# Kernel tuning notes

Hardware: AMD Instinct MI355X
Metric: run time of the kernel (lower is better)

## Reference

```python
import jax, jax.numpy as jnp
import numpy as np

GRID_MIN = -2.0
GRID_MAX = 2.0
NUM_GRIDS = 8
IN_DIM = 512
OUT_DIM = 512
N = 16384
SPLINE_SCALE = 0.1


def setup_inputs() -> dict:
    key = jax.random.key(0)
    k_x, k_sw, k_w, k_b = jax.random.split(key, 4)
    x = jax.random.normal(k_x, (N, IN_DIM), dtype=jnp.float32)
    grid = jnp.linspace(GRID_MIN, GRID_MAX, NUM_GRIDS, dtype=jnp.float32)
    spline_weight = jax.random.normal(k_sw, (IN_DIM * NUM_GRIDS, OUT_DIM), dtype=jnp.float32) * SPLINE_SCALE
    bound = 1.0 / np.sqrt(IN_DIM)
    base_w = jax.random.uniform(k_w, (OUT_DIM, IN_DIM), minval=-bound, maxval=bound, dtype=jnp.float32)
    base_b = jax.random.uniform(k_b, (OUT_DIM,), minval=-bound, maxval=bound, dtype=jnp.float32)
    return {"x": x, "grid": grid, "spline_weight": spline_weight, "base_w": base_w, "base_b": base_b}


def reference(x, grid, spline_weight, base_w, base_b):
    # Gaussian RBF basis over the grid: (N, in_dim, num_grids)
    h = (GRID_MAX - GRID_MIN) / (NUM_GRIDS - 1)  # grid spacing
    basis = jnp.exp(-(((x[..., None] - grid) / h) ** 2))
    ret = basis.reshape(x.shape[0], -1) @ spline_weight  # (N, out_dim)
    base = jax.nn.silu(x) @ base_w.T + base_b
    return ret + base
```

## Files before the change

kernel.cpp:

```cpp
#include <hip/hip_runtime.h>
#include <hip/hip_bf16.h>

typedef __attribute__((ext_vector_type(8))) short short8;
typedef __attribute__((ext_vector_type(4))) float floatx4;

#define N_ROWS   16384
#define IN_DIM   512
#define OUT_DIM  512
#define K_SPLINE 4096
#define K_TOT    4608
#define BM       64
#define BN       256
#define BK       64
#define NKT      (K_TOT / BK)
#define NKTILE   (K_TOT / 32)
#define L2E      1.4426950408889634f
#define C2E      0.13533528323661270f

__device__ __forceinline__ unsigned short f2bf(float f) {
    unsigned int u = __float_as_uint(f);
    unsigned int r = u + 0x7FFFu + ((u >> 16) & 1u);
    return (unsigned short)(r >> 16);
}

__device__ __forceinline__ unsigned pack2bf(float f0, float f1) {
    unsigned u0 = __float_as_uint(f0) + 0x8000u;
    unsigned u1 = __float_as_uint(f1) + 0x8000u;
    return __builtin_amdgcn_perm(u1, u0, 0x07060302);
}

__global__ __launch_bounds__(256) void prep_kernel(
    const float* __restrict__ sw, const float* __restrict__ bw,
    unsigned short* __restrict__ Btf)
{
    const int t     = threadIdx.x;
    const int lane  = t & 63;
    const int ktile = blockIdx.x * 4 + (t >> 6);
    const int ct    = blockIdx.y;
    const int mn    = lane & 15, q = lane >> 4;
    const int n     = ct * 16 + mn;
    const int kbase = ktile * 32 + q * 8;
    short8 v;
    if (kbase < K_SPLINE) {
        #pragma unroll
        for (int j = 0; j < 8; ++j)
            v[j] = (short)f2bf(sw[(size_t)(kbase + j) * OUT_DIM + n]);
    } else {
        #pragma unroll
        for (int j = 0; j < 8; ++j)
            v[j] = (short)f2bf(bw[(size_t)n * IN_DIM + (kbase + j - K_SPLINE)]);
    }
    reinterpret_cast<short8*>(Btf)[(size_t)(ct * NKTILE + ktile) * 64 + lane] = v;
}

__device__ __forceinline__ void stageA(unsigned short* dst, const float* xrow,
                                       int rowA, int colq, int kt)
{
    unsigned short* arow = dst + rowA * 64;
    if (kt < K_SPLINE / BK) {
        const float2 xv = *reinterpret_cast<const float2*>(xrow + kt * 8 + colq * 2);
        #pragma unroll
        for (int e = 0; e < 2; ++e) {
            const float X = e ? xv.y : xv.x;
            const float u = fmaf(1.75f, X, 3.5f);
            float b = __builtin_amdgcn_exp2f(-(u * u) * L2E);
            float r = __builtin_amdgcn_exp2f(fmaf(2.0f * L2E, u, -L2E));
            float v[8];
            v[0] = b;
            #pragma unroll
            for (int j = 1; j < 8; ++j) { b *= r; r *= C2E; v[j] = b; }
            uint4 p;
            p.x = pack2bf(v[0], v[1]);
            p.y = pack2bf(v[2], v[3]);
            p.z = pack2bf(v[4], v[5]);
            p.w = pack2bf(v[6], v[7]);
            const int blk = (colq * 2 + e) ^ (rowA & 7);
            *reinterpret_cast<uint4*>(arow + blk * 8) = p;
        }
    } else {
        const float* xs = xrow + (kt - K_SPLINE / BK) * 64 + colq * 16;
        const float4 a0 = *reinterpret_cast<const float4*>(xs);
        const float4 a1 = *reinterpret_cast<const float4*>(xs + 4);
        const float4 a2 = *reinterpret_cast<const float4*>(xs + 8);
        const float4 a3 = *reinterpret_cast<const float4*>(xs + 12);
        const float f[16] = {a0.x, a0.y, a0.z, a0.w, a1.x, a1.y, a1.z, a1.w,
                             a2.x, a2.y, a2.z, a2.w, a3.x, a3.y, a3.z, a3.w};
        float s[16];
        #pragma unroll
        for (int j = 0; j < 16; ++j)
            s[j] = f[j] * __builtin_amdgcn_rcpf(
                1.0f + __builtin_amdgcn_exp2f(-f[j] * L2E));
        #pragma unroll
        for (int e = 0; e < 2; ++e) {
            uint4 p;
            p.x = pack2bf(s[e * 8 + 0], s[e * 8 + 1]);
            p.y = pack2bf(s[e * 8 + 2], s[e * 8 + 3]);
            p.z = pack2bf(s[e * 8 + 4], s[e * 8 + 5]);
            p.w = pack2bf(s[e * 8 + 6], s[e * 8 + 7]);
            const int blk = (colq * 2 + e) ^ (rowA & 7);
            *reinterpret_cast<uint4*>(arow + blk * 8) = p;
        }
    }
}

template<bool PREP>
__device__ __forceinline__ void load_bfrags(short8 dst[4][2], const short8* __restrict__ Bf,
                                            const size_t* bbase, int kt,
                                            const float* __restrict__ sw,
                                            const float* __restrict__ bw,
                                            int col0, int wn, int lane)
{
    if (PREP) {
        #pragma unroll
        for (int nt = 0; nt < 4; ++nt)
            #pragma unroll
            for (int s = 0; s < 2; ++s)
                dst[nt][s] = Bf[bbase[nt] + (size_t)(kt * 2 + s) * 64];
    } else {
        const int mn = lane & 15, q = lane >> 4;
        #pragma unroll
        for (int nt = 0; nt < 4; ++nt) {
            const int n = col0 + wn * 64 + nt * 16 + mn;
            #pragma unroll
            for (int s = 0; s < 2; ++s) {
                short8 v;
                #pragma unroll
                for (int j = 0; j < 8; ++j) {
                    const int k = (kt * 2 + s) * 32 + q * 8 + j;
                    const float val = (k < K_SPLINE)
                        ? sw[(size_t)k * OUT_DIM + n]
                        : bw[(size_t)n * IN_DIM + (k - K_SPLINE)];
                    v[j] = (short)f2bf(val);
                }
                dst[nt][s] = v;
            }
        }
    }
}

template<bool PREP>
__global__ __launch_bounds__(256, 2) void kan_kernel(
    const float* __restrict__ x,
    const unsigned short* __restrict__ Btf,
    const float* __restrict__ sw,
    const float* __restrict__ bw,
    const float* __restrict__ bias,
    float* __restrict__ out)
{
    __shared__ unsigned short Als[2][BM * BK];

    const int tid  = threadIdx.x;
    const int wn   = tid >> 6;
    const int lane = tid & 63;
    const int q    = lane >> 4;
    const int mn   = lane & 15;
    const int row0 = blockIdx.x * BM;
    const int col0 = blockIdx.y * BN;
    const int rowA = tid >> 2;
    const int colq = tid & 3;

    const float* xrow = x + (size_t)(row0 + rowA) * IN_DIM;

    size_t bbase[4];
    #pragma unroll
    for (int nt = 0; nt < 4; ++nt)
        bbase[nt] = (size_t)(((col0 >> 4) + wn * 4 + nt) * NKTILE) * 64 + lane;
    const short8* Bf = reinterpret_cast<const short8*>(Btf);

    floatx4 acc[4][4];
    #pragma unroll
    for (int i = 0; i < 4; ++i)
        #pragma unroll
        for (int j = 0; j < 4; ++j)
            acc[i][j] = (floatx4){0.f, 0.f, 0.f, 0.f};

    short8 bb[2][4][2];

    stageA(&Als[0][0], xrow, rowA, colq, 0);
    load_bfrags<PREP>(bb[0], Bf, bbase, 0, sw, bw, col0, wn, lane);
    __syncthreads();

    for (int ktb = 0; ktb < NKT; ktb += 2) {
        #pragma unroll
        for (int half = 0; half < 2; ++half) {
            const int kt  = ktb + half;
            const int cur = half;
            const int nxt = half ^ 1;
            if (kt + 1 < NKT) {
                load_bfrags<PREP>(bb[nxt], Bf, bbase, kt + 1, sw, bw, col0, wn, lane);
                stageA(&Als[nxt][0], xrow, rowA, colq, kt + 1);
            }
            #pragma unroll
            for (int s = 0; s < 2; ++s) {
                short8 af[4];
                #pragma unroll
                for (int mt = 0; mt < 4; ++mt) {
                    const int r = mt * 16 + mn;
                    af[mt] = *reinterpret_cast<const short8*>(
                        &Als[cur][r * 64 + (((s * 4 + q) ^ (r & 7)) * 8)]);
                }
                #pragma unroll
                for (int mt = 0; mt < 4; ++mt)
                    #pragma unroll
                    for (int nt = 0; nt < 4; ++nt)
                        acc[mt][nt] = __builtin_amdgcn_mfma_f32_16x16x32_bf16(
                            af[mt], bb[cur][nt][s], acc[mt][nt], 0, 0, 0);
            }
            __syncthreads();
        }
    }

    #pragma unroll
    for (int nt = 0; nt < 4; ++nt) {
        const int col = col0 + wn * 64 + nt * 16 + mn;
        const float bv = bias[col];
        #pragma unroll
        for (int mt = 0; mt < 4; ++mt) {
            const int rb = row0 + mt * 16 + q * 4;
            #pragma unroll
            for (int e = 0; e < 4; ++e)
                out[(size_t)(rb + e) * OUT_DIM + col] = acc[mt][nt][e] + bv;
        }
    }
}

extern "C" void kernel_launch(void* const* d_in, const int* in_sizes, int n_in,
                              void* d_out, int out_size, void* d_ws, size_t ws_size,
                              hipStream_t stream)
{
    const float* x    = (const float*)d_in[0];
    const float* sw   = (const float*)d_in[2];
    const float* bw   = (const float*)d_in[3];
    const float* bias = (const float*)d_in[4];
    float* out = (float*)d_out;

    const size_t bt_bytes = (size_t)OUT_DIM * K_TOT * sizeof(unsigned short);
    if (ws_size >= bt_bytes) {
        unsigned short* Btf = (unsigned short*)d_ws;
        prep_kernel<<<dim3(NKTILE / 4, OUT_DIM / 16), 256, 0, stream>>>(sw, bw, Btf);
        kan_kernel<true><<<dim3(N_ROWS / BM, OUT_DIM / BN), 256, 0, stream>>>(
            x, Btf, sw, bw, bias, out);
    } else {
        kan_kernel<false><<<dim3(N_ROWS / BM, OUT_DIM / BN), 256, 0, stream>>>(
            x, nullptr, sw, bw, bias, out);
    }
}
```

Measured before the change: 174.4 us.

## Generate A fragments in registers per wave, dropping LDS staging and barriers

The shared-memory A tile and its __syncthreads are removed. Each wave now computes the Gaussian basis and SiLU values straight into its MFMA A-operand registers, reading x directly from global memory with a register double buffer. This removes LDS traffic and block-wide synchronisation, but every wave recomputes the same 64 rows' basis, which roughly quadruples exp and VALU work per block. The bf16 packing also switches from round-to-nearest to truncation, which drops a few ALU ops at some cost in accuracy.

Result: slower. 282.6 us (+62.0%).

```diff
diff --git a/kernel.cpp b/kernel.cpp
--- a/kernel.cpp
+++ b/kernel.cpp
@@ -9,10 +9,8 @@
 #define OUT_DIM  512
 #define K_SPLINE 4096
 #define K_TOT    4608
-#define BM       64
-#define BN       256
-#define BK       64
-#define NKT      (K_TOT / BK)
+#define NKT      (K_TOT / 64)
+#define NSPL     (K_SPLINE / 64)
 #define NKTILE   (K_TOT / 32)
 #define L2E      1.4426950408889634f
 #define C2E      0.13533528323661270f
@@ -23,10 +21,41 @@
     return (unsigned short)(r >> 16);
 }
 
-__device__ __forceinline__ unsigned pack2bf(float f0, float f1) {
-    unsigned u0 = __float_as_uint(f0) + 0x8000u;
-    unsigned u1 = __float_as_uint(f1) + 0x8000u;
-    return __builtin_amdgcn_perm(u1, u0, 0x07060302);
+__device__ __forceinline__ unsigned packtrunc(float f0, float f1) {
+    return __builtin_amdgcn_perm(__float_as_uint(f1), __float_as_uint(f0), 0x07060302);
+}
+
+__device__ __forceinline__ short8 gen_basis(float X) {
+    const float u = fmaf(1.75f, X, 3.5f);
+    float b = __builtin_amdgcn_exp2f(-(u * u) * L2E);
+    float r = __builtin_amdgcn_exp2f(fmaf(2.0f * L2E, u, -L2E));
+    float v[8];
+    v[0] = b;
+    #pragma unroll
+    for (int j = 1; j < 8; ++j) { b *= r; r *= C2E; v[j] = b; }
+    union { unsigned d[4]; short8 s; } o;
+    o.d[0] = packtrunc(v[0], v[1]);
+    o.d[1] = packtrunc(v[2], v[3]);
+    o.d[2] = packtrunc(v[4], v[5]);
+    o.d[3] = packtrunc(v[6], v[7]);
+    return o.s;
+}
+
+__device__ __forceinline__ short8 gen_silu(const float* p) {
+    const float4 a0 = *reinterpret_cast<const float4*>(p);
+    const float4 a1 = *reinterpret_cast<const float4*>(p + 4);
+    const float f[8] = {a0.x, a0.y, a0.z, a0.w, a1.x, a1.y, a1.z, a1.w};
+    float s[8];
+    #pragma unroll
+    for (int j = 0; j < 8; ++j)
+        s[j] = f[j] * __builtin_amdgcn_rcpf(
+            1.0f + __builtin_amdgcn_exp2f(-f[j] * L2E));
+    union { unsigned d[4]; short8 v; } o;
+    o.d[0] = packtrunc(s[0], s[1]);
+    o.d[1] = packtrunc(s[2], s[3]);
+    o.d[2] = packtrunc(s[4], s[5]);
+    o.d[3] = packtrunc(s[6], s[7]);
+    return o.v;
 }
 
 __global__ __launch_bounds__(256) void prep_kernel(
@@ -53,62 +82,12 @@
     reinterpret_cast<short8*>(Btf)[(size_t)(ct * NKTILE + ktile) * 64 + lane] = v;
 }
 
-__device__ __forceinline__ void stageA(unsigned short* dst, const float* xrow,
-                                       int rowA, int colq, int kt)
-{
-    unsigned short* arow = dst + rowA * 64;
-    if (kt < K_SPLINE / BK) {
-        const float2 xv = *reinterpret_cast<const float2*>(xrow + kt * 8 + colq * 2);
-        #pragma unroll
-        for (int e = 0; e < 2; ++e) {
-            const float X = e ? xv.y : xv.x;
-            const float u = fmaf(1.75f, X, 3.5f);
-            float b = __builtin_amdgcn_exp2f(-(u * u) * L2E);
-            float r = __builtin_amdgcn_exp2f(fmaf(2.0f * L2E, u, -L2E));
-            float v[8];
-            v[0] = b;
-            #pragma unroll
-            for (int j = 1; j < 8; ++j) { b *= r; r *= C2E; v[j] = b; }
-            uint4 p;
-            p.x = pack2bf(v[0], v[1]);
-            p.y = pack2bf(v[2], v[3]);
-            p.z = pack2bf(v[4], v[5]);
-            p.w = pack2bf(v[6], v[7]);
-            const int blk = (colq * 2 + e) ^ (rowA & 7);
-            *reinterpret_cast<uint4*>(arow + blk * 8) = p;
-        }
-    } else {
-        const float* xs = xrow + (kt - K_SPLINE / BK) * 64 + colq * 16;
-        const float4 a0 = *reinterpret_cast<const float4*>(xs);
-        const float4 a1 = *reinterpret_cast<const float4*>(xs + 4);
-        const float4 a2 = *reinterpret_cast<const float4*>(xs + 8);
-        const float4 a3 = *reinterpret_cast<const float4*>(xs + 12);
-        const float f[16] = {a0.x, a0.y, a0.z, a0.w, a1.x, a1.y, a1.z, a1.w,
-                             a2.x, a2.y, a2.z, a2.w, a3.x, a3.y, a3.z, a3.w};
-        float s[16];
-        #pragma unroll
-        for (int j = 0; j < 16; ++j)
-            s[j] = f[j] * __builtin_amdgcn_rcpf(
-                1.0f + __builtin_amdgcn_exp2f(-f[j] * L2E));
-        #pragma unroll
-        for (int e = 0; e < 2; ++e) {
-            uint4 p;
-            p.x = pack2bf(s[e * 8 + 0], s[e * 8 + 1]);
-            p.y = pack2bf(s[e * 8 + 2], s[e * 8 + 3]);
-            p.z = pack2bf(s[e * 8 + 4], s[e * 8 + 5]);
-            p.w = pack2bf(s[e * 8 + 6], s[e * 8 + 7]);
-            const int blk = (colq * 2 + e) ^ (rowA & 7);
-            *reinterpret_cast<uint4*>(arow + blk * 8) = p;
-        }
-    }
-}
-
 template<bool PREP>
 __device__ __forceinline__ void load_bfrags(short8 dst[4][2], const short8* __restrict__ Bf,
                                             const size_t* bbase, int kt,
                                             const float* __restrict__ sw,
                                             const float* __restrict__ bw,
-                                            int col0, int wn, int lane)
+                                            int col0, int lane)
 {
     if (PREP) {
         #pragma unroll
@@ -120,7 +99,7 @@
         const int mn = lane & 15, q = lane >> 4;
         #pragma unroll
         for (int nt = 0; nt < 4; ++nt) {
-            const int n = col0 + wn * 64 + nt * 16 + mn;
+            const int n = col0 + nt * 16 + mn;
             #pragma unroll
             for (int s = 0; s < 2; ++s) {
                 short8 v;
@@ -147,25 +126,26 @@
     const float* __restrict__ bias,
     float* __restrict__ out)
 {
-    __shared__ unsigned short Als[2][BM * BK];
-
     const int tid  = threadIdx.x;
-    const int wn   = tid >> 6;
+    const int wv   = tid >> 6;
     const int lane = tid & 63;
     const int q    = lane >> 4;
     const int mn   = lane & 15;
-    const int row0 = blockIdx.x * BM;
-    const int col0 = blockIdx.y * BN;
-    const int rowA = tid >> 2;
-    const int colq = tid & 3;
-
-    const float* xrow = x + (size_t)(row0 + rowA) * IN_DIM;
-
+    const int bid  = blockIdx.x;
+    const int half = bid & 1;
+    const int row0 = (bid >> 1) * 64;
+    const int col0 = half * 256 + wv * 64;
+
+    const short8* Bf = reinterpret_cast<const short8*>(Btf);
     size_t bbase[4];
     #pragma unroll
     for (int nt = 0; nt < 4; ++nt)
-        bbase[nt] = (size_t)(((col0 >> 4) + wn * 4 + nt) * NKTILE) * 64 + lane;
-    const short8* Bf = reinterpret_cast<const short8*>(Btf);
+        bbase[nt] = (size_t)(((col0 >> 4) + nt) * NKTILE) * 64 + lane;
+
+    const float* xr[4];
+    #pragma unroll
+    for (int mt = 0; mt < 4; ++mt)
+        xr[mt] = x + (size_t)(row0 + mt * 16 + mn) * IN_DIM;
 
     floatx4 acc[4][4];
     #pragma unroll
@@ -175,44 +155,64 @@
             acc[i][j] = (floatx4){0.f, 0.f, 0.f, 0.f};
 
     short8 bb[2][4][2];
-
-    stageA(&Als[0][0], xrow, rowA, colq, 0);
-    load_bfrags<PREP>(bb[0], Bf, bbase, 0, sw, bw, col0, wn, lane);
-    __syncthreads();
-
-    for (int ktb = 0; ktb < NKT; ktb += 2) {
-        #pragma unroll
-        for (int half = 0; half < 2; ++half) {
-            const int kt  = ktb + half;
-            const int cur = half;
-            const int nxt = half ^ 1;
-            if (kt + 1 < NKT) {
-                load_bfrags<PREP>(bb[nxt], Bf, bbase, kt + 1, sw, bw, col0, wn, lane);
-                stageA(&Als[nxt][0], xrow, rowA, colq, kt + 1);
+    float  xs[2][4][2];
+
+    load_bfrags<PREP>(bb[0], Bf, bbase, 0, sw, bw, col0, lane);
+    #pragma unroll
+    for (int mt = 0; mt < 4; ++mt)
+        #pragma unroll
+        for (int s = 0; s < 2; ++s)
+            xs[0][mt][s] = xr[mt][s * 4 + q];
+
+    for (int ktb = 0; ktb < NSPL; ktb += 2) {
+        #pragma unroll
+        for (int h = 0; h < 2; ++h) {
+            const int kt = ktb + h;
+            const int cur = h, nxt = h ^ 1;
+            load_bfrags<PREP>(bb[nxt], Bf, bbase, kt + 1, sw, bw, col0, lane);
+            if (kt + 1 < NSPL) {
+                #pragma unroll
+                for (int mt = 0; mt < 4; ++mt)
+                    #pragma unroll
+                    for (int s = 0; s < 2; ++s)
+                        xs[nxt][mt][s] = xr[mt][(kt + 1) * 8 + s * 4 + q];
             }
             #pragma unroll
-            for (int s = 0; s < 2; ++s) {
-                short8 af[4];
+            for (int s = 0; s < 2; ++s)
                 #pragma unroll
                 for (int mt = 0; mt < 4; ++mt) {
-                    const int r = mt * 16 + mn;
-                    af[mt] = *reinterpret_cast<const short8*>(
-                        &Als[cur][r * 64 + (((s * 4 + q) ^ (r & 7)) * 8)]);
-                }
-                #pragma unroll
-                for (int mt = 0; mt < 4; ++mt)
+                    const short8 af = gen_basis(xs[cur][mt][s]);
                     #pragma unroll
                     for (int nt = 0; nt < 4; ++nt)
                         acc[mt][nt] = __builtin_amdgcn_mfma_f32_16x16x32_bf16(
-                            af[mt], bb[cur][nt][s], acc[mt][nt], 0, 0, 0);
-            }
-            __syncthreads();
+                            af, bb[cur][nt][s], acc[mt][nt], 0, 0, 0);
+                }
+        }
+    }
+
+    for (int ktb = NSPL; ktb < NKT; ktb += 2) {
+        #pragma unroll
+        for (int h = 0; h < 2; ++h) {
+            const int kt = ktb + h;
+            const int cur = h, nxt = h ^ 1;
+            if (kt + 1 < NKT)
+                load_bfrags<PREP>(bb[nxt], Bf, bbase, kt + 1, sw, bw, col0, lane);
+            #pragma unroll
+            for (int s = 0; s < 2; ++s)
+                #pragma unroll
+                for (int mt = 0; mt < 4; ++mt) {
+                    const short8 af = gen_silu(xr[mt] + (kt - NSPL) * 64 + s * 32 + q * 8);
+                    #pragma unroll
+                    for (int nt = 0; nt < 4; ++nt)
+                        acc[mt][nt] = __builtin_amdgcn_mfma_f32_16x16x32_bf16(
+                            af, bb[cur][nt][s], acc[mt][nt], 0, 0, 0);
+                }
         }
     }
 
     #pragma unroll
     for (int nt = 0; nt < 4; ++nt) {
-        const int col = col0 + wn * 64 + nt * 16 + mn;
+        const int col = col0 + nt * 16 + mn;
         const float bv = bias[col];
         #pragma unroll
         for (int mt = 0; mt < 4; ++mt) {
@@ -238,10 +238,8 @@
     if (ws_size >= bt_bytes) {
         unsigned short* Btf = (unsigned short*)d_ws;
         prep_kernel<<<dim3(NKTILE / 4, OUT_DIM / 16), 256, 0, stream>>>(sw, bw, Btf);
-        kan_kernel<true><<<dim3(N_ROWS / BM, OUT_DIM / BN), 256, 0, stream>>>(
-            x, Btf, sw, bw, bias, out);
+        kan_kernel<true><<<dim3(512), 256, 0, stream>>>(x, Btf, sw, bw, bias, out);
     } else {
-        kan_kernel<false><<<dim3(N_ROWS / BM, OUT_DIM / BN), 256, 0, stream>>>(
-            x, nullptr, sw, bw, bias, out);
-    }
-}
+        kan_kernel<false><<<dim3(512), 256, 0, stream>>>(x, nullptr, sw, bw, bias, out);
+    }
+}
```

## Split K across two warp groups per block with shared-memory reduction

Applied to the files above, without the earlier changes.

Each block now runs 512 threads as two 256-thread halves. Each half computes the same 64x256 output tile over its own half of the K range, and the partial sums are combined through shared memory at the end. B fragments now load one 32-wide k-slice at a time and are interleaved with the MFMAs, and x for the spline path is prefetched a step ahead. The bf16 pack switches from round-to-nearest to truncation. The aim is to raise waves in flight and hide latency on the long K loop, at the cost of a reduction epilogue, larger launch bounds that pressure registers, and slightly lower precision.

Result: slower. 218.4 us (+25.3%).

```diff
diff --git a/kernel.cpp b/kernel.cpp
--- a/kernel.cpp
+++ b/kernel.cpp
@@ -9,11 +9,10 @@
 #define OUT_DIM  512
 #define K_SPLINE 4096
 #define K_TOT    4608
-#define BM       64
-#define BN       256
-#define BK       64
-#define NKT      (K_TOT / BK)
-#define NKTILE   (K_TOT / 32)
+#define NKT      72
+#define KHT      36
+#define NSPL     64
+#define NKTILE   144
 #define L2E      1.4426950408889634f
 #define C2E      0.13533528323661270f
 
@@ -23,10 +22,8 @@
     return (unsigned short)(r >> 16);
 }
 
-__device__ __forceinline__ unsigned pack2bf(float f0, float f1) {
-    unsigned u0 = __float_as_uint(f0) + 0x8000u;
-    unsigned u1 = __float_as_uint(f1) + 0x8000u;
-    return __builtin_amdgcn_perm(u1, u0, 0x07060302);
+__device__ __forceinline__ unsigned packtrunc(float f0, float f1) {
+    return __builtin_amdgcn_perm(__float_as_uint(f1), __float_as_uint(f0), 0x07060302);
 }
 
 __global__ __launch_bounds__(256) void prep_kernel(
@@ -35,11 +32,11 @@
 {
     const int t     = threadIdx.x;
     const int lane  = t & 63;
-    const int ktile = blockIdx.x * 4 + (t >> 6);
+    const int kt32  = blockIdx.x * 4 + (t >> 6);
     const int ct    = blockIdx.y;
     const int mn    = lane & 15, q = lane >> 4;
     const int n     = ct * 16 + mn;
-    const int kbase = ktile * 32 + q * 8;
+    const int kbase = kt32 * 32 + q * 8;
     short8 v;
     if (kbase < K_SPLINE) {
         #pragma unroll
@@ -50,96 +47,93 @@
         for (int j = 0; j < 8; ++j)
             v[j] = (short)f2bf(bw[(size_t)n * IN_DIM + (kbase + j - K_SPLINE)]);
     }
-    reinterpret_cast<short8*>(Btf)[(size_t)(ct * NKTILE + ktile) * 64 + lane] = v;
-}
-
-__device__ __forceinline__ void stageA(unsigned short* dst, const float* xrow,
-                                       int rowA, int colq, int kt)
-{
-    unsigned short* arow = dst + rowA * 64;
-    if (kt < K_SPLINE / BK) {
-        const float2 xv = *reinterpret_cast<const float2*>(xrow + kt * 8 + colq * 2);
-        #pragma unroll
-        for (int e = 0; e < 2; ++e) {
-            const float X = e ? xv.y : xv.x;
-            const float u = fmaf(1.75f, X, 3.5f);
-            float b = __builtin_amdgcn_exp2f(-(u * u) * L2E);
-            float r = __builtin_amdgcn_exp2f(fmaf(2.0f * L2E, u, -L2E));
-            float v[8];
-            v[0] = b;
-            #pragma unroll
-            for (int j = 1; j < 8; ++j) { b *= r; r *= C2E; v[j] = b; }
-            uint4 p;
-            p.x = pack2bf(v[0], v[1]);
-            p.y = pack2bf(v[2], v[3]);
-            p.z = pack2bf(v[4], v[5]);
-            p.w = pack2bf(v[6], v[7]);
-            const int blk = (colq * 2 + e) ^ (rowA & 7);
-            *reinterpret_cast<uint4*>(arow + blk * 8) = p;
-        }
-    } else {
-        const float* xs = xrow + (kt - K_SPLINE / BK) * 64 + colq * 16;
-        const float4 a0 = *reinterpret_cast<const float4*>(xs);
-        const float4 a1 = *reinterpret_cast<const float4*>(xs + 4);
-        const float4 a2 = *reinterpret_cast<const float4*>(xs + 8);
-        const float4 a3 = *reinterpret_cast<const float4*>(xs + 12);
-        const float f[16] = {a0.x, a0.y, a0.z, a0.w, a1.x, a1.y, a1.z, a1.w,
-                             a2.x, a2.y, a2.z, a2.w, a3.x, a3.y, a3.z, a3.w};
-        float s[16];
-        #pragma unroll
-        for (int j = 0; j < 16; ++j)
-            s[j] = f[j] * __builtin_amdgcn_rcpf(
-                1.0f + __builtin_amdgcn_exp2f(-f[j] * L2E));
-        #pragma unroll
-        for (int e = 0; e < 2; ++e) {
-            uint4 p;
-            p.x = pack2bf(s[e * 8 + 0], s[e * 8 + 1]);
-            p.y = pack2bf(s[e * 8 + 2], s[e * 8 + 3]);
-            p.z = pack2bf(s[e * 8 + 4], s[e * 8 + 5]);
-            p.w = pack2bf(s[e * 8 + 6], s[e * 8 + 7]);
-            const int blk = (colq * 2 + e) ^ (rowA & 7);
-            *reinterpret_cast<uint4*>(arow + blk * 8) = p;
-        }
+    reinterpret_cast<short8*>(Btf)[(size_t)(ct * NKTILE + kt32) * 64 + lane] = v;
+}
+
+__device__ __forceinline__ void stage_spline(unsigned short* buf, int rowA, int colq,
+                                             float2 xv)
+{
+    unsigned short* arow = buf + rowA * 64;
+    #pragma unroll
+    for (int e = 0; e < 2; ++e) {
+        const float X = e ? xv.y : xv.x;
+        const float u = fmaf(1.75f, X, 3.5f);
+        float b = __builtin_amdgcn_exp2f(-(u * u) * L2E);
+        float r = __builtin_amdgcn_exp2f(fmaf(2.0f * L2E, u, -L2E));
+        float v[8];
+        v[0] = b;
+        #pragma unroll
+        for (int j = 1; j < 8; ++j) { b *= r; r *= C2E; v[j] = b; }
+        uint4 p;
+        p.x = packtrunc(v[0], v[1]);
+        p.y = packtrunc(v[2], v[3]);
+        p.z = packtrunc(v[4], v[5]);
+        p.w = packtrunc(v[6], v[7]);
+        const int blk = (colq * 2 + e) ^ (rowA & 7);
+        *reinterpret_cast<uint4*>(arow + blk * 8) = p;
+    }
+}
+
+__device__ __forceinline__ void stage_silu(unsigned short* buf, int rowA, int colq,
+                                           const float* xrow, int ktg)
+{
+    unsigned short* arow = buf + rowA * 64;
+    const float* xs = xrow + (ktg - NSPL) * 64 + colq * 16;
+    const float4 a0 = *reinterpret_cast<const float4*>(xs);
+    const float4 a1 = *reinterpret_cast<const float4*>(xs + 4);
+    const float4 a2 = *reinterpret_cast<const float4*>(xs + 8);
+    const float4 a3 = *reinterpret_cast<const float4*>(xs + 12);
+    const float f[16] = {a0.x, a0.y, a0.z, a0.w, a1.x, a1.y, a1.z, a1.w,
+                         a2.x, a2.y, a2.z, a2.w, a3.x, a3.y, a3.z, a3.w};
+    float s[16];
+    #pragma unroll
+    for (int j = 0; j < 16; ++j)
+        s[j] = f[j] * __builtin_amdgcn_rcpf(
+            1.0f + __builtin_amdgcn_exp2f(-f[j] * L2E));
+    #pragma unroll
+    for (int e = 0; e < 2; ++e) {
+        uint4 p;
+        p.x = packtrunc(s[e * 8 + 0], s[e * 8 + 1]);
+        p.y = packtrunc(s[e * 8 + 2], s[e * 8 + 3]);
+        p.z = packtrunc(s[e * 8 + 4], s[e * 8 + 5]);
+        p.w = packtrunc(s[e * 8 + 6], s[e * 8 + 7]);
+        const int blk = (colq * 2 + e) ^ (rowA & 7);
+        *reinterpret_cast<uint4*>(arow + blk * 8) = p;
     }
 }
 
 template<bool PREP>
-__device__ __forceinline__ void load_bfrags(short8 dst[4][2], const short8* __restrict__ Bf,
-                                            const size_t* bbase, int kt,
-                                            const float* __restrict__ sw,
-                                            const float* __restrict__ bw,
-                                            int col0, int wn, int lane)
+__device__ __forceinline__ void loadB(short8 dst[4], const short8* __restrict__ bfp,
+                                      int kt32,
+                                      const float* __restrict__ sw,
+                                      const float* __restrict__ bw,
+                                      int col0, int lane)
 {
     if (PREP) {
         #pragma unroll
         for (int nt = 0; nt < 4; ++nt)
-            #pragma unroll
-            for (int s = 0; s < 2; ++s)
-                dst[nt][s] = Bf[bbase[nt] + (size_t)(kt * 2 + s) * 64];
+            dst[nt] = bfp[(size_t)nt * NKTILE * 64 + (size_t)kt32 * 64];
     } else {
         const int mn = lane & 15, q = lane >> 4;
         #pragma unroll
         for (int nt = 0; nt < 4; ++nt) {
-            const int n = col0 + wn * 64 + nt * 16 + mn;
+            const int n = col0 + nt * 16 + mn;
+            short8 v;
             #pragma unroll
-            for (int s = 0; s < 2; ++s) {
-                short8 v;
-                #pragma unroll
-                for (int j = 0; j < 8; ++j) {
-                    const int k = (kt * 2 + s) * 32 + q * 8 + j;
-                    const float val = (k < K_SPLINE)
-                        ? sw[(size_t)k * OUT_DIM + n]
-                        : bw[(size_t)n * IN_DIM + (k - K_SPLINE)];
-                    v[j] = (short)f2bf(val);
-                }
-                dst[nt][s] = v;
-            }
+            for (int j = 0; j < 8; ++j) {
+                const int k = kt32 * 32 + q * 8 + j;
+                const float val = (k < K_SPLINE)
+                    ? sw[(size_t)k * OUT_DIM + n]
+                    : bw[(size_t)n * IN_DIM + (k - K_SPLINE)];
+                v[j] = (short)f2bf(val);
+            }
+            dst[nt] = v;
         }
     }
 }
 
 template<bool PREP>
-__global__ __launch_bounds__(256, 2) void kan_kernel(
+__global__ __launch_bounds__(512, 4) void kan_kernel(
     const float* __restrict__ x,
     const unsigned short* __restrict__ Btf,
     const float* __restrict__ sw,
@@ -147,25 +141,27 @@
     const float* __restrict__ bias,
     float* __restrict__ out)
 {
-    __shared__ unsigned short Als[2][BM * BK];
+    __shared__ unsigned short Als[2][2][64 * 64];
 
     const int tid  = threadIdx.x;
-    const int wn   = tid >> 6;
+    const int kh   = tid >> 8;
+    const int wn   = (tid >> 6) & 3;
     const int lane = tid & 63;
     const int q    = lane >> 4;
     const int mn   = lane & 15;
-    const int row0 = blockIdx.x * BM;
-    const int col0 = blockIdx.y * BN;
-    const int rowA = tid >> 2;
-    const int colq = tid & 3;
-
-    const float* xrow = x + (size_t)(row0 + rowA) * IN_DIM;
-
-    size_t bbase[4];
-    #pragma unroll
-    for (int nt = 0; nt < 4; ++nt)
-        bbase[nt] = (size_t)(((col0 >> 4) + wn * 4 + nt) * NKTILE) * 64 + lane;
-    const short8* Bf = reinterpret_cast<const short8*>(Btf);
+    const int bid  = blockIdx.x;
+    const int row0 = (bid >> 1) * 64;
+    const int col0 = (bid & 1) * 256 + wn * 64;
+
+    const int th   = tid & 255;
+    const int rowA = th >> 2;
+    const int colq = th & 3;
+    const float* xrowA = x + (size_t)(row0 + rowA) * IN_DIM;
+
+    const short8* Bf  = reinterpret_cast<const short8*>(Btf);
+    const short8* bfp = Bf + (size_t)(col0 >> 4) * NKTILE * 64 + lane;
+
+    const int base = kh * KHT;
 
     floatx4 acc[4][4];
     #pragma unroll
@@ -174,52 +170,114 @@
         for (int j = 0; j < 4; ++j)
             acc[i][j] = (floatx4){0.f, 0.f, 0.f, 0.f};
 
-    short8 bb[2][4][2];
-
-    stageA(&Als[0][0], xrow, rowA, colq, 0);
-    load_bfrags<PREP>(bb[0], Bf, bbase, 0, sw, bw, col0, wn, lane);
+    short8 b0[4], b1[4];
+
+    {
+        const float2 xv = *reinterpret_cast<const float2*>(xrowA + base * 8 + colq * 2);
+        stage_spline(&Als[kh][0][0], rowA, colq, xv);
+    }
+    loadB<PREP>(b0, bfp, base * 2 + 0, sw, bw, col0, lane);
+    loadB<PREP>(b1, bfp, base * 2 + 1, sw, bw, col0, lane);
+    float2 xp = *reinterpret_cast<const float2*>(xrowA + (base + 1) * 8 + colq * 2);
     __syncthreads();
 
-    for (int ktb = 0; ktb < NKT; ktb += 2) {
-        #pragma unroll
-        for (int half = 0; half < 2; ++half) {
-            const int kt  = ktb + half;
-            const int cur = half;
-            const int nxt = half ^ 1;
-            if (kt + 1 < NKT) {
-                load_bfrags<PREP>(bb[nxt], Bf, bbase, kt + 1, sw, bw, col0, wn, lane);
-                stageA(&Als[nxt][0], xrow, rowA, colq, kt + 1);
-            }
-            #pragma unroll
-            for (int s = 0; s < 2; ++s) {
+    for (int ktb = 0; ktb < KHT; ktb += 2) {
+        #pragma unroll
+        for (int h = 0; h < 2; ++h) {
+            const int ktl = ktb + h;
+            const int ktg = base + ktl;
+            const unsigned short* Acur = &Als[kh][h][0];
+            unsigned short*       Anxt = &Als[kh][h ^ 1][0];
+
+            if (ktl + 1 < KHT) {
+                if (ktg + 1 < NSPL) {
+                    stage_spline(Anxt, rowA, colq, xp);
+                    if (ktl + 2 < KHT && ktg + 2 < NSPL)
+                        xp = *reinterpret_cast<const float2*>(
+                            xrowA + (ktg + 2) * 8 + colq * 2);
+                } else {
+                    stage_silu(Anxt, rowA, colq, xrowA, ktg + 1);
+                }
+            }
+
+            {
                 short8 af[4];
                 #pragma unroll
                 for (int mt = 0; mt < 4; ++mt) {
                     const int r = mt * 16 + mn;
                     af[mt] = *reinterpret_cast<const short8*>(
-                        &Als[cur][r * 64 + (((s * 4 + q) ^ (r & 7)) * 8)]);
+                        Acur + r * 64 + ((q ^ (r & 7)) * 8));
                 }
                 #pragma unroll
                 for (int mt = 0; mt < 4; ++mt)
                     #pragma unroll
                     for (int nt = 0; nt < 4; ++nt)
                         acc[mt][nt] = __builtin_amdgcn_mfma_f32_16x16x32_bf16(
-                            af[mt], bb[cur][nt][s], acc[mt][nt], 0, 0, 0);
-            }
+                            af[mt], b0[nt], acc[mt][nt], 0, 0, 0);
+            }
+            if (ktl + 1 < KHT)
+                loadB<PREP>(b0, bfp, (ktg + 1) * 2 + 0, sw, bw, col0, lane);
+
+            {
+                short8 af[4];
+                #pragma unroll
+                for (int mt = 0; mt < 4; ++mt) {
+                    const int r = mt * 16 + mn;
+                    af[mt] = *reinterpret_cast<const short8*>(
+                        Acur + r * 64 + (((4 + q) ^ (r & 7)) * 8));
+                }
+                #pragma unroll
+                for (int mt = 0; mt < 4; ++mt)
+                    #pragma unroll
+                    for (int nt = 0; nt < 4; ++nt)
+                        acc[mt][nt] = __builtin_amdgcn_mfma_f32_16x16x32_bf16(
+                            af[mt], b1[nt], acc[mt][nt], 0, 0, 0);
+            }
+            if (ktl + 1 < KHT)
+                loadB<PREP>(b1, bfp, (ktg + 1) * 2 + 1, sw, bw, col0, lane);
+
             __syncthreads();
         }
     }
 
-    #pragma unroll
-    for (int nt = 0; nt < 4; ++nt) {
-        const int col = col0 + wn * 64 + nt * 16 + mn;
-        const float bv = bias[col];
-        #pragma unroll
-        for (int mt = 0; mt < 4; ++mt) {
-            const int rb = row0 + mt * 16 + q * 4;
+    float* red = reinterpret_cast<float*>(&Als[0][0][0]);
+    #pragma unroll
+    for (int r = 0; r < 2; ++r) {
+        __syncthreads();
+        if (kh == 1) {
             #pragma unroll
-            for (int e = 0; e < 4; ++e)
-                out[(size_t)(rb + e) * OUT_DIM + col] = acc[mt][nt][e] + bv;
+            for (int mtl = 0; mtl < 2; ++mtl)
+                #pragma unroll
+                for (int nt = 0; nt < 4; ++nt)
+                    *reinterpret_cast<floatx4*>(
+                        &red[wn * 2048 + (mtl * 4 + nt) * 256 + lane * 4]) =
+                        acc[r * 2 + mtl][nt];
+        }
+        __syncthreads();
+        if (kh == 0) {
+            #pragma unroll
+            for (int mtl = 0; mtl < 2; ++mtl)
+                #pragma unroll
+                for (int nt = 0; nt < 4; ++nt) {
+                    const floatx4 v = *reinterpret_cast<const floatx4*>(
+                        &red[wn * 2048 + (mtl * 4 + nt) * 256 + lane * 4]);
+                    acc[r * 2 + mtl][nt] += v;
+                }
+        }
+    }
+
+    if (kh == 0) {
+        #pragma unroll
+        for (int nt = 0; nt < 4; ++nt) {
+            const int col = col0 + nt * 16 + mn;
+            const float bv = bias[col];
+            #pragma unroll
+            for (int mt = 0; mt < 4; ++mt) {
+                const int rb = row0 + mt * 16 + q * 4;
+                #pragma unroll
+                for (int e = 0; e < 4; ++e)
+                    out[(size_t)(rb + e) * OUT_DIM + col] = acc[mt][nt][e] + bv;
+            }
         }
     }
 }
@@ -238,10 +296,8 @@
     if (ws_size >= bt_bytes) {
         unsigned short* Btf = (unsigned short*)d_ws;
         prep_kernel<<<dim3(NKTILE / 4, OUT_DIM / 16), 256, 0, stream>>>(sw, bw, Btf);
-        kan_kernel<true><<<dim3(N_ROWS / BM, OUT_DIM / BN), 256, 0, stream>>>(
-            x, Btf, sw, bw, bias, out);
+        kan_kernel<true><<<dim3(512), 512, 0, stream>>>(x, Btf, sw, bw, bias, out);
     } else {
-        kan_kernel<false><<<dim3(N_ROWS / BM, OUT_DIM / BN), 256, 0, stream>>>(
-            x, nullptr, sw, bw, bias, out);
-    }
-}
+        kan_kernel<false><<<dim3(512), 512, 0, stream>>>(x, nullptr, sw, bw, bias, out);
+    }
+}
```

## Split K across two blocks with partial-sum reduce kernel and truncating bf16 pack

Applied to the files above, without the earlier changes.

Splits the K dimension into two halves, each computed by a separate block into an fp32 partial buffer, followed by a reduce kernel that sums the partials and adds the bias. Blocks are now indexed so that adjacent block IDs share a row tile across the two column halves, which is meant to improve reuse of A in cache. The bf16 packing changes from round-to-nearest to truncation, saving ALU work in the staging of A. In exchange it writes and reads two full 32 MB partial buffers, adds a third launch, and lowers the precision of the basis values.

Result: slower. 193.8 us (+11.1%).

```diff
diff --git a/kernel.cpp b/kernel.cpp
--- a/kernel.cpp
+++ b/kernel.cpp
@@ -9,11 +9,10 @@
 #define OUT_DIM  512
 #define K_SPLINE 4096
 #define K_TOT    4608
-#define BM       64
-#define BN       256
-#define BK       64
-#define NKT      (K_TOT / BK)
-#define NKTILE   (K_TOT / 32)
+#define NKT      72
+#define KHT      36
+#define NSPL     64
+#define NKTILE   144
 #define L2E      1.4426950408889634f
 #define C2E      0.13533528323661270f
 
@@ -23,10 +22,8 @@
     return (unsigned short)(r >> 16);
 }
 
-__device__ __forceinline__ unsigned pack2bf(float f0, float f1) {
-    unsigned u0 = __float_as_uint(f0) + 0x8000u;
-    unsigned u1 = __float_as_uint(f1) + 0x8000u;
-    return __builtin_amdgcn_perm(u1, u0, 0x07060302);
+__device__ __forceinline__ unsigned packtrunc(float f0, float f1) {
+    return __builtin_amdgcn_perm(__float_as_uint(f1), __float_as_uint(f0), 0x07060302);
 }
 
 __global__ __launch_bounds__(256) void prep_kernel(
@@ -35,11 +32,11 @@
 {
     const int t     = threadIdx.x;
     const int lane  = t & 63;
-    const int ktile = blockIdx.x * 4 + (t >> 6);
+    const int kt32  = blockIdx.x * 4 + (t >> 6);
     const int ct    = blockIdx.y;
     const int mn    = lane & 15, q = lane >> 4;
     const int n     = ct * 16 + mn;
-    const int kbase = ktile * 32 + q * 8;
+    const int kbase = kt32 * 32 + q * 8;
     short8 v;
     if (kbase < K_SPLINE) {
         #pragma unroll
@@ -50,14 +47,14 @@
         for (int j = 0; j < 8; ++j)
             v[j] = (short)f2bf(bw[(size_t)n * IN_DIM + (kbase + j - K_SPLINE)]);
     }
-    reinterpret_cast<short8*>(Btf)[(size_t)(ct * NKTILE + ktile) * 64 + lane] = v;
+    reinterpret_cast<short8*>(Btf)[(size_t)(ct * NKTILE + kt32) * 64 + lane] = v;
 }
 
 __device__ __forceinline__ void stageA(unsigned short* dst, const float* xrow,
                                        int rowA, int colq, int kt)
 {
     unsigned short* arow = dst + rowA * 64;
-    if (kt < K_SPLINE / BK) {
+    if (kt < NSPL) {
         const float2 xv = *reinterpret_cast<const float2*>(xrow + kt * 8 + colq * 2);
         #pragma unroll
         for (int e = 0; e < 2; ++e) {
@@ -70,15 +67,15 @@
             #pragma unroll
             for (int j = 1; j < 8; ++j) { b *= r; r *= C2E; v[j] = b; }
             uint4 p;
-            p.x = pack2bf(v[0], v[1]);
-            p.y = pack2bf(v[2], v[3]);
-            p.z = pack2bf(v[4], v[5]);
-            p.w = pack2bf(v[6], v[7]);
+            p.x = packtrunc(v[0], v[1]);
+            p.y = packtrunc(v[2], v[3]);
+            p.z = packtrunc(v[4], v[5]);
+            p.w = packtrunc(v[6], v[7]);
             const int blk = (colq * 2 + e) ^ (rowA & 7);
             *reinterpret_cast<uint4*>(arow + blk * 8) = p;
         }
     } else {
-        const float* xs = xrow + (kt - K_SPLINE / BK) * 64 + colq * 16;
+        const float* xs = xrow + (kt - NSPL) * 64 + colq * 16;
         const float4 a0 = *reinterpret_cast<const float4*>(xs);
         const float4 a1 = *reinterpret_cast<const float4*>(xs + 4);
         const float4 a2 = *reinterpret_cast<const float4*>(xs + 8);
@@ -93,10 +90,10 @@
         #pragma unroll
         for (int e = 0; e < 2; ++e) {
             uint4 p;
-            p.x = pack2bf(s[e * 8 + 0], s[e * 8 + 1]);
-            p.y = pack2bf(s[e * 8 + 2], s[e * 8 + 3]);
-            p.z = pack2bf(s[e * 8 + 4], s[e * 8 + 5]);
-            p.w = pack2bf(s[e * 8 + 6], s[e * 8 + 7]);
+            p.x = packtrunc(s[e * 8 + 0], s[e * 8 + 1]);
+            p.y = packtrunc(s[e * 8 + 2], s[e * 8 + 3]);
+            p.z = packtrunc(s[e * 8 + 4], s[e * 8 + 5]);
+            p.w = packtrunc(s[e * 8 + 6], s[e * 8 + 7]);
             const int blk = (colq * 2 + e) ^ (rowA & 7);
             *reinterpret_cast<uint4*>(arow + blk * 8) = p;
         }
@@ -108,7 +105,7 @@
                                             const size_t* bbase, int kt,
                                             const float* __restrict__ sw,
                                             const float* __restrict__ bw,
-                                            int col0, int wn, int lane)
+                                            int col0, int lane)
 {
     if (PREP) {
         #pragma unroll
@@ -120,7 +117,7 @@
         const int mn = lane & 15, q = lane >> 4;
         #pragma unroll
         for (int nt = 0; nt < 4; ++nt) {
-            const int n = col0 + wn * 64 + nt * 16 + mn;
+            const int n = col0 + nt * 16 + mn;
             #pragma unroll
             for (int s = 0; s < 2; ++s) {
                 short8 v;
@@ -138,33 +135,38 @@
     }
 }
 
-template<bool PREP>
+template<bool PREP, bool SPLIT>
 __global__ __launch_bounds__(256, 2) void kan_kernel(
     const float* __restrict__ x,
     const unsigned short* __restrict__ Btf,
     const float* __restrict__ sw,
     const float* __restrict__ bw,
     const float* __restrict__ bias,
-    float* __restrict__ out)
-{
-    __shared__ unsigned short Als[2][BM * BK];
+    float* __restrict__ out,
+    float* __restrict__ Pws)
+{
+    __shared__ unsigned short Als[2][64 * 64];
 
     const int tid  = threadIdx.x;
     const int wn   = tid >> 6;
     const int lane = tid & 63;
     const int q    = lane >> 4;
     const int mn   = lane & 15;
-    const int row0 = blockIdx.x * BM;
-    const int col0 = blockIdx.y * BN;
+    const int bid  = blockIdx.x;
+    const int kh   = SPLIT ? blockIdx.y : 0;
+    const int row0 = (bid >> 1) * 64;
+    const int col0 = (bid & 1) * 256 + wn * 64;
+    const int base = kh * KHT;
+    const int ITER = SPLIT ? KHT : NKT;
+
     const int rowA = tid >> 2;
     const int colq = tid & 3;
-
     const float* xrow = x + (size_t)(row0 + rowA) * IN_DIM;
 
     size_t bbase[4];
     #pragma unroll
     for (int nt = 0; nt < 4; ++nt)
-        bbase[nt] = (size_t)(((col0 >> 4) + wn * 4 + nt) * NKTILE) * 64 + lane;
+        bbase[nt] = (size_t)(((col0 >> 4) + nt) * NKTILE) * 64 + lane;
     const short8* Bf = reinterpret_cast<const short8*>(Btf);
 
     floatx4 acc[4][4];
@@ -176,19 +178,20 @@
 
     short8 bb[2][4][2];
 
-    stageA(&Als[0][0], xrow, rowA, colq, 0);
-    load_bfrags<PREP>(bb[0], Bf, bbase, 0, sw, bw, col0, wn, lane);
+    stageA(&Als[0][0], xrow, rowA, colq, base);
+    load_bfrags<PREP>(bb[0], Bf, bbase, base, sw, bw, col0, lane);
     __syncthreads();
 
-    for (int ktb = 0; ktb < NKT; ktb += 2) {
+    for (int ktb = 0; ktb < ITER; ktb += 2) {
         #pragma unroll
         for (int half = 0; half < 2; ++half) {
-            const int kt  = ktb + half;
+            const int ktl = ktb + half;
+            const int ktg = base + ktl;
             const int cur = half;
             const int nxt = half ^ 1;
-            if (kt + 1 < NKT) {
-                load_bfrags<PREP>(bb[nxt], Bf, bbase, kt + 1, sw, bw, col0, wn, lane);
-                stageA(&Als[nxt][0], xrow, rowA, colq, kt + 1);
+            if (ktl + 1 < ITER) {
+                load_bfrags<PREP>(bb[nxt], Bf, bbase, ktg + 1, sw, bw, col0, lane);
+                stageA(&Als[nxt][0], xrow, rowA, colq, ktg + 1);
             }
             #pragma unroll
             for (int s = 0; s < 2; ++s) {
@@ -210,18 +213,35 @@
         }
     }
 
+    float* dst = SPLIT ? (Pws + (size_t)kh * N_ROWS * OUT_DIM) : out;
     #pragma unroll
     for (int nt = 0; nt < 4; ++nt) {
-        const int col = col0 + wn * 64 + nt * 16 + mn;
-        const float bv = bias[col];
+        const int col = col0 + nt * 16 + mn;
+        const float bv = SPLIT ? 0.0f : bias[col];
         #pragma unroll
         for (int mt = 0; mt < 4; ++mt) {
             const int rb = row0 + mt * 16 + q * 4;
             #pragma unroll
             for (int e = 0; e < 4; ++e)
-                out[(size_t)(rb + e) * OUT_DIM + col] = acc[mt][nt][e] + bv;
-        }
-    }
+                dst[(size_t)(rb + e) * OUT_DIM + col] = acc[mt][nt][e] + bv;
+        }
+    }
+}
+
+__global__ __launch_bounds__(256) void reduce_kernel(
+    const float* __restrict__ Pws, const float* __restrict__ bias,
+    float* __restrict__ out)
+{
+    const size_t idx = ((size_t)blockIdx.x * 256 + threadIdx.x) * 4;
+    const float4 p0 = *reinterpret_cast<const float4*>(Pws + idx);
+    const float4 p1 = *reinterpret_cast<const float4*>(Pws + (size_t)N_ROWS * OUT_DIM + idx);
+    const float4 bv = *reinterpret_cast<const float4*>(bias + (idx & (OUT_DIM - 1)));
+    float4 o;
+    o.x = p0.x + p1.x + bv.x;
+    o.y = p0.y + p1.y + bv.y;
+    o.z = p0.z + p1.z + bv.z;
+    o.w = p0.w + p1.w + bv.w;
+    *reinterpret_cast<float4*>(out + idx) = o;
 }
 
 extern "C" void kernel_launch(void* const* d_in, const int* in_sizes, int n_in,
@@ -235,13 +255,23 @@
     float* out = (float*)d_out;
 
     const size_t bt_bytes = (size_t)OUT_DIM * K_TOT * sizeof(unsigned short);
-    if (ws_size >= bt_bytes) {
+    const size_t p_bytes  = (size_t)2 * N_ROWS * OUT_DIM * sizeof(float);
+
+    if (ws_size >= bt_bytes + p_bytes) {
+        unsigned short* Btf = (unsigned short*)d_ws;
+        float* Pws = (float*)((char*)d_ws + bt_bytes);
+        prep_kernel<<<dim3(NKTILE / 4, OUT_DIM / 16), 256, 0, stream>>>(sw, bw, Btf);
+        kan_kernel<true, true><<<dim3(512, 2), 256, 0, stream>>>(
+            x, Btf, sw, bw, bias, out, Pws);
+        reduce_kernel<<<dim3(N_ROWS * OUT_DIM / 4 / 256), 256, 0, stream>>>(
+            Pws, bias, out);
+    } else if (ws_size >= bt_bytes) {
         unsigned short* Btf = (unsigned short*)d_ws;
         prep_kernel<<<dim3(NKTILE / 4, OUT_DIM / 16), 256, 0, stream>>>(sw, bw, Btf);
-        kan_kernel<true><<<dim3(N_ROWS / BM, OUT_DIM / BN), 256, 0, stream>>>(
-            x, Btf, sw, bw, bias, out);
-    } else {
-        kan_kernel<false><<<dim3(N_ROWS / BM, OUT_DIM / BN), 256, 0, stream>>>(
-            x, nullptr, sw, bw, bias, out);
-    }
-}
+        kan_kernel<true, false><<<dim3(512), 256, 0, stream>>>(
+            x, Btf, sw, bw, bias, out, nullptr);
+    } else {
+        kan_kernel<false, false><<<dim3(512), 256, 0, stream>>>(
+            x, nullptr, sw, bw, bias, out, nullptr);
+    }
+}
```
